# Kernel tuning notes

Measured on AMD Instinct MI355X. Metric: run time of the kernel, lower is better.

The kernel has to match this reference:

```python
import jax, jax.numpy as jnp
import numpy as np
from itertools import product

B = 2
X, Y, Z = 96, 96, 192          # voxel grid (x, y, t)
NPB = 300_000                   # occupied voxels per batch item
PX, PY, PZ = X // 2, Y // 2, Z // 4  # pooled grid (kernel/stride [2,2,4])
CIN, COUT, KVOL, NCONV = 32, 64, 27, 2
EPS = 1e-5


def _build_maps():
    """Builds sparse coordinates, maxpool segment ids and 3x3x3 conv kernel maps
    (gather/scatter index pairs per kernel offset), mirroring MinkowskiEngine's
    coordinate manager."""
    rng = np.random.default_rng(0)
    coords = []
    for b in range(B):
        lin = rng.choice(X * Y * Z, NPB, replace=False)
        x = lin // (Y * Z)
        y = (lin // Z) % Y
        z = lin % Z
        coords.append(np.stack([np.full(NPB, b), x, y, z], 1))
    c = np.concatenate(coords).astype(np.int64)  # [N,4] (b,x,y,z)
    # max-pool coord map: out coord = (x//2, y//2, z//4)
    pk = ((c[:, 0] * PX + c[:, 1] // 2) * PY + c[:, 2] // 2) * PZ + c[:, 3] // 4
    uniq, inv = np.unique(pk, return_inverse=True)
    M = len(uniq)
    pz = uniq % PZ
    py = (uniq // PZ) % PY
    px = (uniq // (PZ * PY)) % PX
    pb = uniq // (PZ * PY * PX)
    lut = np.full(B * PX * PY * PZ, -1, np.int64)
    lut[uniq] = np.arange(M)
    ins, outs = [], []
    for dx, dy, dz in product((-1, 0, 1), repeat=3):
        nx, ny, nz = px + dx, py + dy, pz + dz
        ok = (nx >= 0) & (nx < PX) & (ny >= 0) & (ny < PY) & (nz >= 0) & (nz < PZ)
        nk = ((pb * PX + np.clip(nx, 0, PX - 1)) * PY + np.clip(ny, 0, PY - 1)) * PZ + np.clip(nz, 0, PZ - 1)
        j = np.where(ok, lut[nk], -1)
        sel = j >= 0
        ins.append(j[sel])
        outs.append(np.arange(M)[sel])
    L = max(len(a) for a in ins)
    ci = np.full((KVOL, L), M, np.int64)  # pad -> index M (zero row)
    co = np.full((KVOL, L), M, np.int64)  # pad -> dummy out row M (dropped)
    for k in range(KVOL):
        ci[k, : len(ins[k])] = ins[k]
        co[k, : len(outs[k])] = outs[k]
    return inv.astype(np.int64), ci, co, M


def setup_inputs() -> dict:
    key = jax.random.key(0)
    ks = jax.random.split(key, 4)
    pool_seg, ci, co, M = _build_maps()
    N = B * NPB
    feats = jax.random.normal(ks[0], (N, CIN), jnp.float32)
    Wd = jax.random.normal(ks[1], (CIN, COUT), jnp.float32) / np.sqrt(CIN)
    W1 = jax.random.normal(ks[2], (KVOL, COUT, COUT), jnp.float32) / np.sqrt(KVOL * COUT)
    W2 = jax.random.normal(ks[3], (KVOL, COUT, COUT), jnp.float32) / np.sqrt(KVOL * COUT)
    ones = jnp.ones((COUT,), jnp.float32)
    zeros = jnp.zeros((COUT,), jnp.float32)
    return {
        "feats": feats, "Wd": Wd,
        "g0": ones, "b0": zeros,
        "W1": W1, "g1": ones, "b1": zeros,
        "W2": W2, "g2": ones, "b2": zeros,
        "pool_seg": jnp.asarray(pool_seg),
        "conv_in": jnp.asarray(ci), "conv_out": jnp.asarray(co),
        "num_pooled": int(M),
    }


def _bn(h, g, b):
    # training-mode batch norm over all sparse points (biased variance, eps=1e-5)
    m = h.mean(0)
    v = jnp.mean((h - m) ** 2, 0)
    return (h - m) * (g / jnp.sqrt(v + EPS)) + b


def _sparse_conv(h, W, conv_in, conv_out, M):
    # gather-GEMM-scatter over 27 kernel offsets (MinkowskiConvolution, bias=False)
    C = W.shape[-1]
    hp = jnp.concatenate([h, jnp.zeros((1, h.shape[1]), h.dtype)])  # zero pad row
    out = jnp.zeros((M + 1, C), h.dtype)
    for k in range(W.shape[0]):
        out = out.at[conv_out[k]].add(hp[conv_in[k]] @ W[k])
    return out[:M]


def reference(feats, Wd, g0, b0, W1, g1, b1, W2, g2, b2,
              pool_seg, conv_in, conv_out, num_pooled):
    # down_conv (1x1, bias=False) -> BN -> ELU
    h = jax.nn.elu(_bn(feats @ Wd, g0, b0))
    # MinkowskiMaxPooling kernel=stride=[2,2,4] == segment max over pooled cells
    down = jax.ops.segment_max(h, pool_seg, num_segments=num_pooled)
    # nConvs LUConv blocks: ELU(BN(conv3x3x3(x)))
    o = down
    for W, g, b in ((W1, g1, b1), (W2, g2, b2)):
        o = jax.nn.elu(_bn(_sparse_conv(o, W, conv_in, conv_out, num_pooled), g, b))
    # residual add + ELU
    return jax.nn.elu(o + down)
```

## Files before the change

### kernel.cpp

```cpp
#include <hip/hip_runtime.h>
#include <math.h>

#define CIN  32
#define COUT 64
#define KVOL 27
#define EPSF 1e-5f

typedef __attribute__((ext_vector_type(8))) short          short8;
typedef __attribute__((ext_vector_type(8))) unsigned short u16x8;
typedef __attribute__((ext_vector_type(4))) float          float4v;

__device__ __forceinline__ float eluf(float x) { return x > 0.f ? x : expm1f(x); }

__device__ __forceinline__ unsigned short f2bf(float x) {
    unsigned u = __float_as_uint(x);
    unsigned r = (u + 0x7FFFu + ((u >> 16) & 1u)) >> 16;
    return (unsigned short)r;
}
__device__ __forceinline__ unsigned pk2bf(float lo, float hi) {
    return (unsigned)f2bf(lo) | ((unsigned)f2bf(hi) << 16);
}
__device__ __forceinline__ float bf2f(unsigned short h) {
    return __uint_as_float(((unsigned)h) << 16);
}

__global__ void prep_kernel(const float* __restrict__ W1, const float* __restrict__ W2,
                            const float* __restrict__ Wd,
                            unsigned short* __restrict__ Wt1, unsigned short* __restrict__ Wt2,
                            unsigned short* __restrict__ Wdt,
                            const int* __restrict__ pool_seg, int* __restrict__ cnt,
                            int* __restrict__ bucket, int N,
                            const int* __restrict__ conv_out, const int* __restrict__ conv_in,
                            int* __restrict__ nbrT, int L, int M, int nbB, int nbL)
{
    int b = blockIdx.x, t = threadIdx.x;
    if (b < 55) {
        if (b == 54) {
            for (int e = t; e < CIN * COUT; e += 256) {
                int i = e >> 6, c = e & 63;
                Wdt[c * CIN + i] = f2bf(Wd[e]);
            }
            return;
        }
        const float* W = (b < 27) ? W1 : W2;
        unsigned short* Wt = (b < 27) ? Wt1 : Wt2;
        int k = (b < 27) ? b : b - 27;
        const float* src = W + (size_t)k * (COUT * COUT);
        unsigned short* dst = Wt + (size_t)k * (COUT * COUT);
        for (int e = t; e < COUT * COUT; e += 256) {
            int i = e >> 6, c = e & 63;
            dst[c * COUT + i] = f2bf(src[e]);
        }
        return;
    }
    b -= 55;
    if (b < nbB) {
        int j = b * 256 + t;
        if (j < N) {
            int s = pool_seg[j];
            int pos = atomicAdd(&cnt[s], 1);
            bucket[(size_t)s * 16 + pos] = j;
        }
        return;
    }
    b -= nbB;
    int k = b / nbL, blk = b - k * nbL;
    int idx = blk * 256 + t;
    if (idx < L) {
        int e = k * L + idx;
        int j = conv_out[e];
        if (j < M) nbrT[(size_t)k * M + j] = conv_in[e];
    }
}

__global__ __launch_bounds__(256) void gemm_t_kernel(
    const float* __restrict__ feats, const unsigned short* __restrict__ Wdt,
    int N, unsigned short* __restrict__ t_bf, float* __restrict__ red0)
{
    __shared__ float red_s[64];
    __shared__ float red_q[64];
    __shared__ __align__(16) unsigned short xpose[4][16 * 64];
    int t = threadIdx.x;
    if (t < 64) { red_s[t] = 0.f; red_q[t] = 0.f; }
    __syncthreads();

    int w = t >> 6, lane = t & 63, l15 = lane & 15, quad = lane >> 4;
    int p = lane >> 2, qq = lane & 3;

    short8 aw[4];
    #pragma unroll
    for (int mt = 0; mt < 4; ++mt)
        aw[mt] = *(const short8*)(Wdt + (size_t)(16 * mt + l15) * CIN + quad * 8);

    float s1[16], sq[16];
    #pragma unroll
    for (int e = 0; e < 16; ++e) { s1[e] = 0.f; sq[e] = 0.f; }

    int numTiles = (N + 15) >> 4;
    int stride = gridDim.x * 4;
    int tile = blockIdx.x * 4 + w;

    float4 c0 = make_float4(0.f, 0.f, 0.f, 0.f), c1 = c0;
    {
        int pt = tile * 16 + l15;
        if (tile < numTiles && pt < N) {
            const float4* s = (const float4*)(feats + (size_t)pt * CIN + quad * 8);
            c0 = s[0]; c1 = s[1];
        }
    }

    while (tile < numTiles) {
        int nt = tile + stride;
        float4 n0 = make_float4(0.f, 0.f, 0.f, 0.f), n1 = n0;
        {
            int npt = nt * 16 + l15;
            if (nt < numTiles && npt < N) {
                const float4* s = (const float4*)(feats + (size_t)npt * CIN + quad * 8);
                n0 = s[0]; n1 = s[1];
            }
        }
        union { short8 v; unsigned u[4]; } b;
        b.u[0] = pk2bf(c0.x, c0.y);
        b.u[1] = pk2bf(c0.z, c0.w);
        b.u[2] = pk2bf(c1.x, c1.y);
        b.u[3] = pk2bf(c1.z, c1.w);

        float4v acc[4];
        #pragma unroll
        for (int mt = 0; mt < 4; ++mt)
            acc[mt] = __builtin_amdgcn_mfma_f32_16x16x32_bf16(
                aw[mt], b.v, (float4v){0.f, 0.f, 0.f, 0.f}, 0, 0, 0);

        {
            char* xb = (char*)xpose[w];
            #pragma unroll
            for (int mt = 0; mt < 4; ++mt) {
                uint2 o;
                o.x = pk2bf(acc[mt][0], acc[mt][1]);
                o.y = pk2bf(acc[mt][2], acc[mt][3]);
                *(uint2*)(xb + l15 * 128 + (((mt * 4 + quad) ^ l15) * 8)) = o;
            }
            int pt2 = tile * 16 + p;
            if (pt2 < N) {
                uint2 d0 = *(uint2*)(xb + p * 128 + (((qq * 4 + 0) ^ p) * 8));
                uint2 d1 = *(uint2*)(xb + p * 128 + (((qq * 4 + 1) ^ p) * 8));
                uint2 d2 = *(uint2*)(xb + p * 128 + (((qq * 4 + 2) ^ p) * 8));
                uint2 d3 = *(uint2*)(xb + p * 128 + (((qq * 4 + 3) ^ p) * 8));
                uint4 o0 = make_uint4(d0.x, d0.y, d1.x, d1.y);
                uint4 o1 = make_uint4(d2.x, d2.y, d3.x, d3.y);
                *(uint4*)(t_bf + (size_t)pt2 * COUT + qq * 16) = o0;
                *(uint4*)(t_bf + (size_t)pt2 * COUT + qq * 16 + 8) = o1;
            }
        }

        #pragma unroll
        for (int mt = 0; mt < 4; ++mt)
            #pragma unroll
            for (int e = 0; e < 4; ++e) {
                float v = acc[mt][e];
                s1[mt * 4 + e] += v; sq[mt * 4 + e] += v * v;
            }
        c0 = n0; c1 = n1;
        tile = nt;
    }

    #pragma unroll
    for (int m = 1; m <= 8; m <<= 1) {
        #pragma unroll
        for (int e = 0; e < 16; ++e) {
            s1[e] += __shfl_xor(s1[e], m);
            sq[e] += __shfl_xor(sq[e], m);
        }
    }
    if (l15 == 0) {
        #pragma unroll
        for (int e = 0; e < 16; ++e) {
            int ch = (e >> 2) * 16 + quad * 4 + (e & 3);
            atomicAdd(&red_s[ch], s1[e]);
            atomicAdd(&red_q[ch], sq[e]);
        }
    }
    __syncthreads();
    float* dst = red0 + (size_t)(blockIdx.x & 3) * 128;
    if (t < 64)       atomicAdd(&dst[t], red_s[t]);
    else if (t < 128) atomicAdd(&dst[t], red_q[t - 64]);
}

__global__ __launch_bounds__(256) void pool_max_kernel(
    const unsigned short* __restrict__ t_bf,
    const int* __restrict__ cnt, const int* __restrict__ bucket,
    const float* __restrict__ red0, const float* __restrict__ g0,
    const float* __restrict__ b0,
    unsigned short* __restrict__ down_bf, int M, int N)
{
    __shared__ float sc_s[64], sh_s[64];
    int t = threadIdx.x;
    if (t < 64) {
        float s = 0.f, q2 = 0.f;
        #pragma unroll
        for (int i = 0; i < 4; ++i) { s += red0[i * 128 + t]; q2 += red0[i * 128 + 64 + t]; }
        float m = s / (float)N;
        float var = q2 / (float)N - m * m;
        float sc = g0[t] / sqrtf(var + EPSF);
        sc_s[t] = sc;
        sh_s[t] = b0[t] - m * sc;
    }
    __syncthreads();

    int id = blockIdx.x * 256 + t;
    int s = id >> 4, cg = id & 15;
    if (s >= M) return;
    int n = cnt[s];
    const int4* bk4 = (const int4*)(bucket + (size_t)s * 16);
    float4 mx = make_float4(-INFINITY, -INFINITY, -INFINITY, -INFINITY);
    float4 mn = make_float4( INFINITY,  INFINITY,  INFINITY,  INFINITY);
    #pragma unroll
    for (int ch = 0; ch < 4; ++ch) {
        if (ch * 4 >= n) break;
        int4 b4 = bk4[ch];
        #pragma unroll
        for (int e = 0; e < 4; ++e) {
            int p = ch * 4 + e;
            if (p < n) {
                int idx = (e == 0) ? b4.x : (e == 1) ? b4.y : (e == 2) ? b4.z : b4.w;
                ushort4 v = *(const ushort4*)(t_bf + (size_t)idx * COUT + cg * 4);
                float f0 = bf2f(v.x), f1 = bf2f(v.y), f2 = bf2f(v.z), f3 = bf2f(v.w);
                mx.x = fmaxf(mx.x, f0); mn.x = fminf(mn.x, f0);
                mx.y = fmaxf(mx.y, f1); mn.y = fminf(mn.y, f1);
                mx.z = fmaxf(mx.z, f2); mn.z = fminf(mn.z, f2);
                mx.w = fmaxf(mx.w, f3); mn.w = fminf(mn.w, f3);
            }
        }
    }
    int c0 = cg * 4;
    float scx = sc_s[c0], scy = sc_s[c0 + 1], scz = sc_s[c0 + 2], scw = sc_s[c0 + 3];
    float shx = sh_s[c0], shy = sh_s[c0 + 1], shz = sh_s[c0 + 2], shw = sh_s[c0 + 3];
    ushort4 o;
    o.x = f2bf(eluf(scx * (scx >= 0.f ? mx.x : mn.x) + shx));
    o.y = f2bf(eluf(scy * (scy >= 0.f ? mx.y : mn.y) + shy));
    o.z = f2bf(eluf(scz * (scz >= 0.f ? mx.z : mn.z) + shz));
    o.w = f2bf(eluf(scw * (scw >= 0.f ? mx.w : mn.w) + shw));
    *(ushort4*)(down_bf + (size_t)s * COUT + c0) = o;
}

__global__ __launch_bounds__(256) void bn_elu_cvt_kernel(
    const unsigned short* __restrict__ o1b, const float* __restrict__ red,
    const float* __restrict__ g, const float* __restrict__ bb,
    unsigned short* __restrict__ o1t, int n4, int M)
{
    __shared__ float sc_s[64], sh_s[64];
    int t = threadIdx.x;
    if (t < 64) {
        float m = red[t] / (float)M;
        float var = red[64 + t] / (float)M - m * m;
        float sc = g[t] / sqrtf(var + EPSF);
        sc_s[t] = sc;
        sh_s[t] = bb[t] - m * sc;
    }
    __syncthreads();
    int i = blockIdx.x * 256 + t;
    if (i < n4) {
        ushort4 v = ((const ushort4*)o1b)[i];
        int c0 = (i & 15) * 4;
        ushort4 o;
        o.x = f2bf(eluf(bf2f(v.x) * sc_s[c0]     + sh_s[c0]));
        o.y = f2bf(eluf(bf2f(v.y) * sc_s[c0 + 1] + sh_s[c0 + 1]));
        o.z = f2bf(eluf(bf2f(v.z) * sc_s[c0 + 2] + sh_s[c0 + 2]));
        o.w = f2bf(eluf(bf2f(v.w) * sc_s[c0 + 3] + sh_s[c0 + 3]));
        ((ushort4*)o1t)[i] = o;
    }
}

__global__ __launch_bounds__(256) void final_kernel(
    float* __restrict__ out, const unsigned short* __restrict__ o2b,
    const unsigned short* __restrict__ down_bf,
    const float* __restrict__ red, const float* __restrict__ g,
    const float* __restrict__ bb, int n4, int M)
{
    __shared__ float sc_s[64], sh_s[64];
    int t = threadIdx.x;
    if (t < 64) {
        float m = red[t] / (float)M;
        float var = red[64 + t] / (float)M - m * m;
        float sc = g[t] / sqrtf(var + EPSF);
        sc_s[t] = sc;
        sh_s[t] = bb[t] - m * sc;
    }
    __syncthreads();
    int i = blockIdx.x * 256 + t;
    if (i < n4) {
        ushort4 v = ((const ushort4*)o2b)[i];
        ushort4 d = ((const ushort4*)down_bf)[i];
        int c0 = (i & 15) * 4;
        float4 o;
        o.x = eluf(eluf(bf2f(v.x) * sc_s[c0]     + sh_s[c0])     + bf2f(d.x));
        o.y = eluf(eluf(bf2f(v.y) * sc_s[c0 + 1] + sh_s[c0 + 1]) + bf2f(d.y));
        o.z = eluf(eluf(bf2f(v.z) * sc_s[c0 + 2] + sh_s[c0 + 2]) + bf2f(d.z));
        o.w = eluf(eluf(bf2f(v.w) * sc_s[c0 + 3] + sh_s[c0 + 3]) + bf2f(d.w));
        ((float4*)out)[i] = o;
    }
}

__global__ __launch_bounds__(512, 4) void conv_mfma_kernel(
    const unsigned short* __restrict__ in, const unsigned short* __restrict__ Wt,
    const int* __restrict__ nbrT, int M,
    unsigned short* __restrict__ outb, float* __restrict__ red_out)
{
    __shared__ __align__(16) unsigned short A_lds[2][256 * 64];
    __shared__ __align__(16) unsigned short W_lds[2][64 * 64];
    int t = threadIdx.x;

    int nwg = gridDim.x;
    int q = nwg >> 3, r = nwg & 7;
    int xcd = blockIdx.x & 7, pos = blockIdx.x >> 3;
    int sb = (xcd < r ? xcd * (q + 1) : r * (q + 1) + (xcd - r) * q) + pos;
    int base = sb * 256;

    int w = t >> 6, lane = t & 63, l15 = lane & 15, quad = lane >> 4;

    int c8 = t & 7, rg = t >> 3;
    int j0 = base + rg;

    float4v acc[2][4];
    #pragma unroll
    for (int s = 0; s < 2; ++s)
        #pragma unroll
        for (int n = 0; n < 4; ++n)
            acc[s][n] = (float4v){0.f, 0.f, 0.f, 0.f};

    int awo = rg * 64 + ((c8 ^ (rg & 7)) * 8);
    int wwo = awo;

    const u16x8 z8 = (u16x8){0, 0, 0, 0, 0, 0, 0, 0};

    {
        int pidx[4];
        #pragma unroll
        for (int m = 0; m < 4; ++m) {
            int j = j0 + 64 * m;
            pidx[m] = (j < M) ? nbrT[j] : -1;
        }
        u16x8 pa[4];
        #pragma unroll
        for (int m = 0; m < 4; ++m)
            pa[m] = (pidx[m] >= 0)
                ? *(const u16x8*)(in + (size_t)pidx[m] * COUT + c8 * 8) : z8;
        u16x8 w0 = *(const u16x8*)(Wt + rg * COUT + c8 * 8);
        #pragma unroll
        for (int m = 0; m < 4; ++m)
            *(u16x8*)(A_lds[0] + awo + m * 4096) = pa[m];
        *(u16x8*)(W_lds[0] + wwo) = w0;
    }
    int nidx[4];
    #pragma unroll
    for (int m = 0; m < 4; ++m) {
        int j = j0 + 64 * m;
        nidx[m] = (j < M) ? nbrT[(size_t)M + j] : -1;
    }
    __syncthreads();

    for (int k = 0; k < KVOL; ++k) {
        int cur = k & 1;
        bool pf = (k + 1 < KVOL);

        u16x8 na[4]; u16x8 nw = z8;
        if (pf) {
            #pragma unroll
            for (int m = 0; m < 4; ++m) {
                na[m] = (nidx[m] >= 0)
                    ? *(const u16x8*)(in + (size_t)nidx[m] * COUT + c8 * 8) : z8;
            }
            nw = *(const u16x8*)(Wt + (size_t)(k + 1) * (COUT * COUT) + rg * COUT + c8 * 8);
            #pragma unroll
            for (int m = 0; m < 4; ++m) {
                int j = j0 + 64 * m;
                nidx[m] = (k + 2 < KVOL && j < M) ? nbrT[(size_t)(k + 2) * M + j] : -1;
            }
        }
        __builtin_amdgcn_sched_barrier(0);

        const unsigned short* Ab = A_lds[cur];
        const unsigned short* Wb = W_lds[cur];
        #pragma unroll
        for (int kk = 0; kk < 64; kk += 32) {
            int slb = quad + (kk >> 3);
            int r0 = 32 * w + l15;
            short8 a0 = *(const short8*)(Ab + r0 * 64 + ((slb ^ (r0 & 7)) * 8));
            int r1 = r0 + 16;
            short8 a1 = *(const short8*)(Ab + r1 * 64 + ((slb ^ (r1 & 7)) * 8));
            #pragma unroll
            for (int n = 0; n < 4; ++n) {
                int rb = 16 * n + l15;
                short8 b = *(const short8*)(Wb + rb * 64 + ((slb ^ (rb & 7)) * 8));
                acc[0][n] = __builtin_amdgcn_mfma_f32_16x16x32_bf16(a0, b, acc[0][n], 0, 0, 0);
                acc[1][n] = __builtin_amdgcn_mfma_f32_16x16x32_bf16(a1, b, acc[1][n], 0, 0, 0);
            }
        }

        if (pf) {
            unsigned short* An = A_lds[cur ^ 1];
            #pragma unroll
            for (int m = 0; m < 4; ++m)
                *(u16x8*)(An + awo + m * 4096) = na[m];
            *(u16x8*)(W_lds[cur ^ 1] + wwo) = nw;
        }
        __syncthreads();
    }

    #pragma unroll
    for (int s = 0; s < 2; ++s) {
        int row = base + 32 * w + 16 * s + quad * 4;
        #pragma unroll
        for (int n = 0; n < 4; ++n) {
            int c = 16 * n + l15;
            #pragma unroll
            for (int e = 0; e < 4; ++e)
                if (row + e < M)
                    outb[(size_t)(row + e) * COUT + c] = f2bf(acc[s][n][e]);
        }
    }

    float* red_s = (float*)(W_lds[0]);
    float* red_q = red_s + 64;
    if (t < 128) red_s[t] = 0.f;
    __syncthreads();
    #pragma unroll
    for (int n = 0; n < 4; ++n) {
        float s1 = 0.f, sq = 0.f;
        #pragma unroll
        for (int s = 0; s < 2; ++s)
            #pragma unroll
            for (int e = 0; e < 4; ++e) { float v = acc[s][n][e]; s1 += v; sq += v * v; }
        s1 += __shfl_xor(s1, 16); sq += __shfl_xor(sq, 16);
        s1 += __shfl_xor(s1, 32); sq += __shfl_xor(sq, 32);
        if (quad == 0) {
            atomicAdd(&red_s[16 * n + l15], s1);
            atomicAdd(&red_q[16 * n + l15], sq);
        }
    }
    __syncthreads();
    if (t < 64)       atomicAdd(&red_out[t], red_s[t]);
    else if (t < 128) atomicAdd(&red_out[t], red_q[t - 64]);
}

extern "C" void kernel_launch(void* const* d_in, const int* in_sizes, int n_in,
                              void* d_out, int out_size, void* d_ws, size_t ws_size,
                              hipStream_t stream)
{
    (void)n_in; (void)ws_size;
    const float* feats    = (const float*)d_in[0];
    const float* Wd       = (const float*)d_in[1];
    const float* g0       = (const float*)d_in[2];
    const float* b0       = (const float*)d_in[3];
    const float* W1       = (const float*)d_in[4];
    const float* g1       = (const float*)d_in[5];
    const float* b1       = (const float*)d_in[6];
    const float* W2       = (const float*)d_in[7];
    const float* g2       = (const float*)d_in[8];
    const float* b2       = (const float*)d_in[9];
    const int*   pool_seg = (const int*)d_in[10];
    const int*   conv_in  = (const int*)d_in[11];
    const int*   conv_out = (const int*)d_in[12];

    int N = in_sizes[0] / CIN;
    int M = out_size / COUT;
    int L = in_sizes[11] / KVOL;

    char* ws = (char*)d_ws;
    size_t off = 0;
    auto alloc = [&](size_t bytes) -> void* {
        void* p = ws + off;
        off = (off + bytes + 255) & ~(size_t)255;
        return p;
    };
    unsigned short* down_bf = (unsigned short*)alloc((size_t)M * COUT * 2);
    unsigned short* o1b     = (unsigned short*)alloc((size_t)M * COUT * 2);
    unsigned short* o1t     = (unsigned short*)alloc((size_t)M * COUT * 2);
    unsigned short* o2b     = (unsigned short*)alloc((size_t)M * COUT * 2);
    unsigned short* t_bf    = (unsigned short*)alloc((size_t)N * COUT * 2);
    int*            nbrT    = (int*)alloc((size_t)KVOL * M * 4);
    unsigned short* Wt1     = (unsigned short*)alloc((size_t)KVOL * COUT * COUT * 2);
    unsigned short* Wt2     = (unsigned short*)alloc((size_t)KVOL * COUT * COUT * 2);
    unsigned short* Wdt     = (unsigned short*)alloc((size_t)CIN * COUT * 2);
    int*            bucket  = (int*)alloc((size_t)M * 16 * 4);
    int*            cnt     = (int*)alloc((size_t)M * 4);
    float*          red     = (float*)alloc((size_t)768 * 4);
    float* red0 = red, *red1 = red + 512, *red2 = red + 640;

    hipMemsetAsync(nbrT, 0xFF, (size_t)KVOL * M * 4, stream);
    hipMemsetAsync(cnt, 0, (size_t)((char*)(red + 768) - (char*)cnt), stream);

    int nbB = (N + 255) / 256, nbL = (L + 255) / 256;
    prep_kernel<<<55 + nbB + nbL * KVOL, 256, 0, stream>>>(
        W1, W2, Wd, Wt1, Wt2, Wdt, pool_seg, cnt, bucket, N,
        conv_out, conv_in, nbrT, L, M, nbB, nbL);
    gemm_t_kernel<<<1024, 256, 0, stream>>>(feats, Wdt, N, t_bf, red0);
    pool_max_kernel<<<(M * 16 + 255) / 256, 256, 0, stream>>>(
        t_bf, cnt, bucket, red0, g0, b0, down_bf, M, N);

    int cblocks = (M + 255) / 256;
    int n4 = (M * COUT) / 4;
    conv_mfma_kernel<<<cblocks, 512, 0, stream>>>(down_bf, Wt1, nbrT, M, o1b, red1);
    bn_elu_cvt_kernel<<<(n4 + 255) / 256, 256, 0, stream>>>(o1b, red1, g1, b1, o1t, n4, M);
    conv_mfma_kernel<<<cblocks, 512, 0, stream>>>(o1t, Wt2, nbrT, M, o2b, red2);
    final_kernel<<<(n4 + 255) / 256, 256, 0, stream>>>(
        (float*)d_out, o2b, down_bf, red2, g2, b2, n4, M);
}
```

Measured before the change: 486.0 us.

## Stage gathered conv rows directly into LDS via global_load_lds

Replaces the register-staged gather (global load into VGPRs, then ds_write) in the sparse conv MFMA kernel with direct global-to-LDS DMA loads. Missing neighbours now point at a zero pad row appended to the input buffers instead of being filled with zeros by a branch. The swizzle is applied on the global-address side, and the thread-to-row mapping is reorganised per wave. This is meant to cut VGPR pressure and LDS write instructions and to overlap the next tap's loads with the MFMAs. It adds two small memsets, and it relies on the per-lane LDS destination layout of global_load_lds matching the swizzled reads.

```diff
diff --git a/kernel.cpp b/kernel.cpp
--- a/kernel.cpp
+++ b/kernel.cpp
@@ -22,6 +22,12 @@
 }
 __device__ __forceinline__ float bf2f(unsigned short h) {
     return __uint_as_float(((unsigned)h) << 16);
+}
+
+__device__ __forceinline__ void gload_lds16(const unsigned short* src, unsigned short* dst) {
+    __builtin_amdgcn_global_load_lds(
+        (const __attribute__((address_space(1))) unsigned int*)(const void*)src,
+        (__attribute__((address_space(3))) unsigned int*)(void*)dst, 16, 0, 0);
 }
 
 __global__ void prep_kernel(const float* __restrict__ W1, const float* __restrict__ W2,
@@ -302,7 +308,8 @@
 }
 
 __global__ __launch_bounds__(512, 4) void conv_mfma_kernel(
-    const unsigned short* __restrict__ in, const unsigned short* __restrict__ Wt,
+    const unsigned short* __restrict__ in,
+    const unsigned short* __restrict__ Wt,
     const int* __restrict__ nbrT, int M,
     unsigned short* __restrict__ outb, float* __restrict__ red_out)
 {
@@ -317,9 +324,7 @@
     int base = sb * 256;
 
     int w = t >> 6, lane = t & 63, l15 = lane & 15, quad = lane >> 4;
-
-    int c8 = t & 7, rg = t >> 3;
-    int j0 = base + rg;
+    int ar8 = lane >> 3, ac = lane & 7;
 
     float4v acc[2][4];
     #pragma unroll
@@ -328,59 +333,45 @@
         for (int n = 0; n < 4; ++n)
             acc[s][n] = (float4v){0.f, 0.f, 0.f, 0.f};
 
-    int awo = rg * 64 + ((c8 ^ (rg & 7)) * 8);
-    int wwo = awo;
-
-    const u16x8 z8 = (u16x8){0, 0, 0, 0, 0, 0, 0, 0};
-
-    {
-        int pidx[4];
-        #pragma unroll
-        for (int m = 0; m < 4; ++m) {
-            int j = j0 + 64 * m;
-            pidx[m] = (j < M) ? nbrT[j] : -1;
-        }
-        u16x8 pa[4];
-        #pragma unroll
-        for (int m = 0; m < 4; ++m)
-            pa[m] = (pidx[m] >= 0)
-                ? *(const u16x8*)(in + (size_t)pidx[m] * COUT + c8 * 8) : z8;
-        u16x8 w0 = *(const u16x8*)(Wt + rg * COUT + c8 * 8);
-        #pragma unroll
-        for (int m = 0; m < 4; ++m)
-            *(u16x8*)(A_lds[0] + awo + m * 4096) = pa[m];
-        *(u16x8*)(W_lds[0] + wwo) = w0;
-    }
-    int nidx[4];
-    #pragma unroll
-    for (int m = 0; m < 4; ++m) {
-        int j = j0 + 64 * m;
-        nidx[m] = (j < M) ? nbrT[(size_t)M + j] : -1;
-    }
+    auto LOADIDX = [&](int k, int* e) {
+        #pragma unroll
+        for (int i = 0; i < 4; ++i) {
+            int rr = (w << 5) + (i << 3) + ar8;
+            int j = base + rr;
+            int idx = nbrT[(size_t)k * M + (j < M ? j : 0)];
+            e[i] = (j < M && idx >= 0) ? idx : M;
+        }
+    };
+    auto STAGE = [&](int buf, const int* e, int kw) {
+        unsigned short* An = A_lds[buf];
+        unsigned short* Wn = W_lds[buf];
+        #pragma unroll
+        for (int i = 0; i < 4; ++i) {
+            int rr = (w << 5) + (i << 3) + ar8;
+            gload_lds16(in + (size_t)e[i] * COUT + ((ac ^ (rr & 7)) * 8),
+                        An + (w << 11) + (i << 9));
+        }
+        int wr = (w << 3) + ar8;
+        gload_lds16(Wt + (size_t)kw * (COUT * COUT) + wr * COUT + ((ac ^ (wr & 7)) * 8),
+                    Wn + (w << 9));
+    };
+
+    int eC[4], eN[4];
+    LOADIDX(0, eC);
+    STAGE(0, eC, 0);
+    LOADIDX(1, eC);
     __syncthreads();
 
     for (int k = 0; k < KVOL; ++k) {
-        int cur = k & 1;
         bool pf = (k + 1 < KVOL);
-
-        u16x8 na[4]; u16x8 nw = z8;
         if (pf) {
-            #pragma unroll
-            for (int m = 0; m < 4; ++m) {
-                na[m] = (nidx[m] >= 0)
-                    ? *(const u16x8*)(in + (size_t)nidx[m] * COUT + c8 * 8) : z8;
-            }
-            nw = *(const u16x8*)(Wt + (size_t)(k + 1) * (COUT * COUT) + rg * COUT + c8 * 8);
-            #pragma unroll
-            for (int m = 0; m < 4; ++m) {
-                int j = j0 + 64 * m;
-                nidx[m] = (k + 2 < KVOL && j < M) ? nbrT[(size_t)(k + 2) * M + j] : -1;
-            }
+            STAGE((k + 1) & 1, eC, k + 1);
+            if (k + 2 < KVOL) LOADIDX(k + 2, eN);
         }
         __builtin_amdgcn_sched_barrier(0);
 
-        const unsigned short* Ab = A_lds[cur];
-        const unsigned short* Wb = W_lds[cur];
+        const unsigned short* Ab = A_lds[k & 1];
+        const unsigned short* Wb = W_lds[k & 1];
         #pragma unroll
         for (int kk = 0; kk < 64; kk += 32) {
             int slb = quad + (kk >> 3);
@@ -398,11 +389,8 @@
         }
 
         if (pf) {
-            unsigned short* An = A_lds[cur ^ 1];
-            #pragma unroll
-            for (int m = 0; m < 4; ++m)
-                *(u16x8*)(An + awo + m * 4096) = na[m];
-            *(u16x8*)(W_lds[cur ^ 1] + wwo) = nw;
+            #pragma unroll
+            for (int i = 0; i < 4; ++i) eC[i] = eN[i];
         }
         __syncthreads();
     }
@@ -473,9 +461,9 @@
         off = (off + bytes + 255) & ~(size_t)255;
         return p;
     };
-    unsigned short* down_bf = (unsigned short*)alloc((size_t)M * COUT * 2);
+    unsigned short* down_bf = (unsigned short*)alloc((size_t)(M + 1) * COUT * 2);
     unsigned short* o1b     = (unsigned short*)alloc((size_t)M * COUT * 2);
-    unsigned short* o1t     = (unsigned short*)alloc((size_t)M * COUT * 2);
+    unsigned short* o1t     = (unsigned short*)alloc((size_t)(M + 1) * COUT * 2);
     unsigned short* o2b     = (unsigned short*)alloc((size_t)M * COUT * 2);
     unsigned short* t_bf    = (unsigned short*)alloc((size_t)N * COUT * 2);
     int*            nbrT    = (int*)alloc((size_t)KVOL * M * 4);
@@ -489,6 +477,8 @@
 
     hipMemsetAsync(nbrT, 0xFF, (size_t)KVOL * M * 4, stream);
     hipMemsetAsync(cnt, 0, (size_t)((char*)(red + 768) - (char*)cnt), stream);
+    hipMemsetAsync(down_bf + (size_t)M * COUT, 0, COUT * 2, stream);
+    hipMemsetAsync(o1t + (size_t)M * COUT, 0, COUT * 2, stream);
 
     int nbB = (N + 255) / 256, nbL = (L + 255) / 256;
     prep_kernel<<<55 + nbB + nbL * KVOL, 256, 0, stream>>>(
```

After: 481.8 us. Within noise of the previous version (-0.9%).
